# Kernel optimization log

Hardware: AMD Instinct MI355X
Metric: run time of the kernel (lower is better)

Reference implementation:

```python
import jax, jax.numpy as jnp
import numpy as np

N_NODES = 50000
N_EDGES = 1600000
F_NODE, F_EDGE, HID = 16, 8, 64


def setup_inputs() -> dict:
    key = jax.random.key(0)
    ks = jax.random.split(key, 12)
    def w(k, shape):
        fan_in = shape[0]
        return jax.random.normal(k, shape, dtype=jnp.float32) / np.sqrt(fan_in)
    return {
        "x": jax.random.normal(ks[0], (N_NODES, F_NODE), dtype=jnp.float32),
        "edge_index": jax.random.randint(ks[1], (2, N_EDGES), 0, N_NODES, dtype=jnp.int32),
        "edge_attr": jax.random.normal(ks[2], (N_EDGES, F_EDGE), dtype=jnp.float32),
        "W1": w(ks[3], (F_NODE, HID)), "b1": jnp.zeros((HID,), jnp.float32),
        "W2": w(ks[4], (HID, HID)), "b2": jnp.zeros((HID,), jnp.float32),
        "mW1": w(ks[5], (2 * HID + F_EDGE, 2 * HID)), "mb1": jnp.zeros((2 * HID,), jnp.float32),
        "mW2": w(ks[6], (2 * HID, HID)), "mb2": jnp.zeros((HID,), jnp.float32),
        "mW3": w(ks[7], (HID, 1)), "mb3": jnp.zeros((1,), jnp.float32),
    }


def _gcn_conv(x, W, b, src, dst, deg_inv_sqrt, n_nodes):
    # GCNConv: D^{-1/2} (A + I) D^{-1/2} X W + b, edges include self-loops
    xw = x @ W  # [N, H]
    norm = deg_inv_sqrt[src] * deg_inv_sqrt[dst]  # [E+N]
    agg = jax.ops.segment_sum(xw[src] * norm[:, None], dst, num_segments=n_nodes)
    return agg + b


def reference(x, edge_index, edge_attr, W1, b1, W2, b2, mW1, mb1, mW2, mb2, mW3, mb3):
    n_nodes = x.shape[0]
    loop = jnp.arange(n_nodes, dtype=edge_index.dtype)
    src = jnp.concatenate([edge_index[0], loop])  # add self-loops
    dst = jnp.concatenate([edge_index[1], loop])
    deg = jax.ops.segment_sum(jnp.ones_like(dst, dtype=x.dtype), dst, num_segments=n_nodes)
    dis = jnp.where(deg > 0, jax.lax.rsqrt(deg), 0.0)

    h = jax.nn.relu(_gcn_conv(x, W1, b1, src, dst, dis, n_nodes))
    h = jax.nn.relu(_gcn_conv(h, W2, b2, src, dst, dis, n_nodes))

    # Vectorized equivalent of the per-graph neighbor loop: Q for every
    # (current_node=src, neighbor=dst) directed edge using its edge_attr.
    h_cur = h[edge_index[0]]   # [E, H]
    h_nbr = h[edge_index[1]]   # [E, H]
    z = jnp.concatenate([h_cur, h_nbr, edge_attr], axis=-1)  # [E, 2H+Fe]
    z = jax.nn.relu(z @ mW1 + mb1)
    z = jax.nn.relu(z @ mW2 + mb2)
    q = (z @ mW3 + mb3)[:, 0]  # [E]
    return q
```

## Files before the change

### kernel.cpp

```cpp
#include <hip/hip_runtime.h>
#include <hip/hip_bf16.h>

#define HID 64
#define FNODE 16
#define FEDGE 8

typedef __bf16 v8bf __attribute__((ext_vector_type(8)));
typedef unsigned short us8 __attribute__((ext_vector_type(8)));
typedef float v4f __attribute__((ext_vector_type(4)));

__device__ __bf16 g_w1h[20480];
__device__ __bf16 g_w1l[20480];
__device__ __bf16 g_w2h[8192];
__device__ __bf16 g_w2l[8192];

__global__ void k_pack(const float* __restrict__ mW1, const float* __restrict__ mW2) {
    int gid = blockIdx.x * 256 + threadIdx.x;
    if (gid < 20480) {
        int j = gid & 7, lane = (gid >> 3) & 63, f = gid >> 9;
        int kt = f >> 3, nt = f & 7;
        int k = kt * 32 + (lane >> 4) * 8 + j;
        int col = nt * 16 + (lane & 15);
        float x = (k < 136) ? mW1[k * 128 + col] : 0.f;
        __bf16 hi = (__bf16)x;
        g_w1h[gid] = hi;
        g_w1l[gid] = (__bf16)(x - (float)hi);
    } else if (gid < 28672) {
        int t = gid - 20480;
        int j = t & 7, lane = (t >> 3) & 63, f = t >> 9;
        int kt = f >> 2, nt = f & 3;
        int k = kt * 32 + (lane >> 4) * 8 + j;
        int col = nt * 16 + (lane & 15);
        float x = mW2[k * 64 + col];
        __bf16 hi = (__bf16)x;
        g_w2h[t] = hi;
        g_w2l[t] = (__bf16)(x - (float)hi);
    }
}

__global__ void k_count(const int* __restrict__ ei, int* __restrict__ rp, int E) {
    int e = blockIdx.x * 256 + threadIdx.x;
    if (e < E) atomicAdd(&rp[ei[E + e]], 1);
}

__global__ void k_disn(const int* __restrict__ rp, float* __restrict__ dis, int N) {
    int n = blockIdx.x * 256 + threadIdx.x;
    if (n < N) dis[n] = rsqrtf((float)(rp[n] + 1));
}

__device__ __forceinline__ int block_scan_excl(int v, int* wsum) {
    int lane = threadIdx.x & 63, wv = threadIdx.x >> 6;
    int inc = v;
#pragma unroll
    for (int d = 1; d < 64; d <<= 1) {
        int t = __shfl_up(inc, d, 64);
        if (lane >= d) inc += t;
    }
    if (lane == 63) wsum[wv] = inc;
    __syncthreads();
    int off = 0;
    for (int w = 0; w < wv; ++w) off += wsum[w];
    return off + inc - v;
}

__global__ void k_scan1(int* __restrict__ rp, int* __restrict__ bsum, int N) {
    __shared__ int ws[4];
    int i = blockIdx.x * 256 + threadIdx.x;
    int v = (i < N) ? rp[i] : 0;
    int excl = block_scan_excl(v, ws);
    if (i < N) rp[i] = excl;
    if (threadIdx.x == 255) bsum[blockIdx.x] = excl + v;
}

__global__ void k_scan2(int* __restrict__ bsum, int nb) {
    __shared__ int ws[4];
    int i = threadIdx.x;
    int v = (i < nb) ? bsum[i] : 0;
    int excl = block_scan_excl(v, ws);
    if (i < nb) bsum[i] = excl;
}

__global__ void k_scan3(int* __restrict__ rp, const int* __restrict__ bsum, int N) {
    int i = blockIdx.x * 256 + threadIdx.x;
    if (i < N) rp[i] += bsum[i >> 8];
}

__global__ void k_fill(const int* __restrict__ ei, int* __restrict__ rp,
                       int* __restrict__ ce, int* __restrict__ eid, int E) {
    int e = blockIdx.x * 256 + threadIdx.x;
    if (e < E) {
        int s = ei[e], d = ei[E + e];
        int pos = atomicAdd(&rp[d], 1);
        ce[pos] = s | (d << 16);
        eid[pos] = e;
    }
}

__global__ void k_dx(const float* __restrict__ x, const float* __restrict__ dis,
                     float* __restrict__ dx, int NF) {
    int t = blockIdx.x * 256 + threadIdx.x;
    if (t < NF) dx[t] = x[t] * dis[t >> 4];
}

__global__ __launch_bounds__(256) void k_pull1x(const float* __restrict__ dx,
                                                const int* __restrict__ rp,
                                                const int* __restrict__ ce,
                                                const float* __restrict__ dis,
                                                float* __restrict__ u, int N) {
    int grp = threadIdx.x >> 4, dim = threadIdx.x & 15;
    int n = blockIdx.x * 16 + grp;
    if (n >= N) return;
    int beg = n ? rp[n - 1] : 0;
    int end = rp[n];
    float a0 = dx[(size_t)n * 16 + dim];
    float a1 = 0.f, a2 = 0.f, a3 = 0.f, a4 = 0.f, a5 = 0.f, a6 = 0.f, a7 = 0.f;
    int j = beg;
    for (; j + 7 < end; j += 8) {
        a0 += dx[(size_t)(ce[j] & 0xffff) * 16 + dim];
        a1 += dx[(size_t)(ce[j + 1] & 0xffff) * 16 + dim];
        a2 += dx[(size_t)(ce[j + 2] & 0xffff) * 16 + dim];
        a3 += dx[(size_t)(ce[j + 3] & 0xffff) * 16 + dim];
        a4 += dx[(size_t)(ce[j + 4] & 0xffff) * 16 + dim];
        a5 += dx[(size_t)(ce[j + 5] & 0xffff) * 16 + dim];
        a6 += dx[(size_t)(ce[j + 6] & 0xffff) * 16 + dim];
        a7 += dx[(size_t)(ce[j + 7] & 0xffff) * 16 + dim];
    }
    for (; j < end; ++j) a0 += dx[(size_t)(ce[j] & 0xffff) * 16 + dim];
    u[(size_t)n * 16 + dim] =
        dis[n] * (((a0 + a1) + (a2 + a3)) + ((a4 + a5) + (a6 + a7)));
}

__global__ __launch_bounds__(256) void k_h1y2(const float* __restrict__ u,
                                              const float* __restrict__ W1,
                                              const float* __restrict__ b1,
                                              const float* __restrict__ W2,
                                              const float* __restrict__ dis,
                                              float* __restrict__ y2, int N) {
    __shared__ float sh[4][64];
    int wave = threadIdx.x >> 6, lane = threadIdx.x & 63;
    int n = blockIdx.x * 4 + wave;
    if (n >= N) return;
    float myu = u[(size_t)n * 16 + (lane & 15)];
    float h = b1[lane];
#pragma unroll
    for (int k = 0; k < 16; ++k)
        h = fmaf(__shfl(myu, k, 64), W1[k * HID + lane], h);
    h = fmaxf(h, 0.f);
    sh[wave][lane] = h;
    float acc = 0.f;
#pragma unroll 8
    for (int k = 0; k < HID; ++k)
        acc = fmaf(sh[wave][k], W2[k * HID + lane], acc);
    y2[(size_t)n * HID + lane] = dis[n] * acc;
}

__global__ __launch_bounds__(256) void k_pull2(const float* __restrict__ y,
                                               const int* __restrict__ rp,
                                               const int* __restrict__ ce,
                                               const float* __restrict__ dis,
                                               const float* __restrict__ b,
                                               __bf16* __restrict__ hp, int N) {
    int wave = threadIdx.x >> 6, lane = threadIdx.x & 63;
    int n = blockIdx.x * 4 + wave;
    if (n >= N) return;
    int beg = n ? rp[n - 1] : 0;
    int end = rp[n];
    float a0 = y[(size_t)n * HID + lane];
    float a1 = 0.f, a2 = 0.f, a3 = 0.f, a4 = 0.f, a5 = 0.f, a6 = 0.f, a7 = 0.f;
    int j = beg;
    for (; j + 7 < end; j += 8) {
        a0 += y[(size_t)(ce[j] & 0xffff) * HID + lane];
        a1 += y[(size_t)(ce[j + 1] & 0xffff) * HID + lane];
        a2 += y[(size_t)(ce[j + 2] & 0xffff) * HID + lane];
        a3 += y[(size_t)(ce[j + 3] & 0xffff) * HID + lane];
        a4 += y[(size_t)(ce[j + 4] & 0xffff) * HID + lane];
        a5 += y[(size_t)(ce[j + 5] & 0xffff) * HID + lane];
        a6 += y[(size_t)(ce[j + 6] & 0xffff) * HID + lane];
        a7 += y[(size_t)(ce[j + 7] & 0xffff) * HID + lane];
    }
    for (; j < end; ++j) a0 += y[(size_t)(ce[j] & 0xffff) * HID + lane];
    float v = fmaxf(
        dis[n] * (((a0 + a1) + (a2 + a3)) + ((a4 + a5) + (a6 + a7))) + b[lane], 0.f);
    __bf16 hi = (__bf16)v;
    __bf16* p = hp + (size_t)n * 128;
    p[lane] = hi;
    p[64 + lane] = (__bf16)(v - (float)hi);
}

__device__ __forceinline__ int zoff(int m, int ch) {
    return ((m >> 4) << 12) + ((ch >> 2) << 9) + ((m & 15) << 5) + ((ch & 3) << 3);
}

__global__ __launch_bounds__(256) void k_edge_mlp(
    const __bf16* __restrict__ hp, const int* __restrict__ ce,
    const int* __restrict__ eid, const float* __restrict__ ea,
    const float* __restrict__ mb1, const float* __restrict__ mb2,
    const float* __restrict__ mW3, const float* __restrict__ mb3,
    float* __restrict__ q, int E) {
    __shared__ __align__(16) __bf16 zc[16384];
    __shared__ __align__(16) __bf16 eh[64][32];
    __shared__ __align__(16) __bf16 el[64][32];

    const int tid = threadIdx.x;
    const int lane = tid & 63;
    const int wave = tid >> 6;
    const int g = lane >> 4;
    const int cb = lane & 15;
    const int m0 = blockIdx.x * 64;

    {
        const int me = wave * 16 + (lane >> 2);
        const int cl = lane & 3;
        const int p = m0 + me;
        const bool valid = p < E;
        const int cep = valid ? ce[p] : 0;
        const int s = cep & 0xffff;
        const int d = ((unsigned)cep) >> 16;
        const __bf16* Sp = hp + (size_t)s * 128 + cl * 8;
        const __bf16* Dp = hp + (size_t)d * 128 + cl * 8;
        __bf16* lb = zc + wave * 4096;
#pragma unroll
        for (int i = 0; i < 4; ++i)
            __builtin_amdgcn_global_load_lds(
                (const __attribute__((address_space(1))) unsigned int*)(Sp + i * 32),
                (__attribute__((address_space(3))) unsigned int*)(lb + i * 512),
                16, 0, 0);
#pragma unroll
        for (int i = 0; i < 4; ++i)
            __builtin_amdgcn_global_load_lds(
                (const __attribute__((address_space(1))) unsigned int*)(Dp + i * 32),
                (__attribute__((address_space(3))) unsigned int*)(lb + (4 + i) * 512),
                16, 0, 0);
    }
    {
        const int m = tid >> 2, qt = tid & 3;
        const int p = m0 + m;
        const bool valid = p < E;
        if (qt < 2) {
            float4 v = {0.f, 0.f, 0.f, 0.f};
            if (valid) {
                int e = eid[p];
                v = *(const float4*)(ea + (size_t)e * FEDGE + qt * 4);
            }
            const float* vf = (const float*)&v;
#pragma unroll
            for (int i2 = 0; i2 < 4; ++i2) {
                float vv = vf[i2];
                __bf16 hiv = (__bf16)vv;
                eh[m][qt * 4 + i2] = hiv;
                el[m][qt * 4 + i2] = (__bf16)(vv - (float)hiv);
            }
        } else {
            us8 zz = {};
            __bf16* dstp = (qt == 2) ? &eh[m][8] : &el[m][8];
            *(us8*)&dstp[0] = zz;
            *(us8*)&dstp[8] = zz;
            *(us8*)&dstp[16] = zz;
        }
    }
    __syncthreads();

    const int nt0 = wave * 2;
    v4f acc[2][4];
    {
        float b0 = mb1[nt0 * 16 + cb];
        float b1v = mb1[nt0 * 16 + 16 + cb];
#pragma unroll
        for (int mt = 0; mt < 4; ++mt) {
            acc[0][mt] = (v4f){b0, b0, b0, b0};
            acc[1][mt] = (v4f){b1v, b1v, b1v, b1v};
        }
    }
    const v8bf* w1h = (const v8bf*)g_w1h;
    const v8bf* w1l = (const v8bf*)g_w1l;
    const v8bf* w2h = (const v8bf*)g_w2h;
    const v8bf* w2l = (const v8bf*)g_w2l;
#pragma unroll
    for (int kt = 0; kt < 5; ++kt) {
        v8bf bh0 = w1h[(kt * 8 + nt0) * 64 + lane];
        v8bf bl0 = w1l[(kt * 8 + nt0) * 64 + lane];
        v8bf bh1 = w1h[(kt * 8 + nt0 + 1) * 64 + lane];
        v8bf bl1 = w1l[(kt * 8 + nt0 + 1) * 64 + lane];
#pragma unroll
        for (int mt = 0; mt < 4; ++mt) {
            v8bf ah, al;
            if (kt < 4) {
                int ch = (kt < 2) ? kt * 4 + g : 16 + (kt - 2) * 4 + g;
                ah = *(const v8bf*)&zc[zoff(mt * 16 + cb, ch)];
                al = *(const v8bf*)&zc[zoff(mt * 16 + cb, ch + 8)];
            } else {
                ah = *(const v8bf*)&eh[mt * 16 + cb][g * 8];
                al = *(const v8bf*)&el[mt * 16 + cb][g * 8];
            }
            acc[0][mt] = __builtin_amdgcn_mfma_f32_16x16x32_bf16(ah, bh0, acc[0][mt], 0, 0, 0);
            acc[0][mt] = __builtin_amdgcn_mfma_f32_16x16x32_bf16(ah, bl0, acc[0][mt], 0, 0, 0);
            acc[0][mt] = __builtin_amdgcn_mfma_f32_16x16x32_bf16(al, bh0, acc[0][mt], 0, 0, 0);
            acc[1][mt] = __builtin_amdgcn_mfma_f32_16x16x32_bf16(ah, bh1, acc[1][mt], 0, 0, 0);
            acc[1][mt] = __builtin_amdgcn_mfma_f32_16x16x32_bf16(ah, bl1, acc[1][mt], 0, 0, 0);
            acc[1][mt] = __builtin_amdgcn_mfma_f32_16x16x32_bf16(al, bh1, acc[1][mt], 0, 0, 0);
        }
    }
    __syncthreads();

#pragma unroll
    for (int c = 0; c < 2; ++c)
#pragma unroll
        for (int mt = 0; mt < 4; ++mt)
#pragma unroll
            for (int r = 0; r < 4; ++r) {
                float vv = fmaxf(acc[c][mt][r], 0.f);
                __bf16 hiv = (__bf16)vv;
                int row = mt * 16 + g * 4 + r;
                int col = (nt0 + c) * 16 + cb;
                int chh = (col < 64) ? (col >> 3) : (8 + (col >> 3));
                zc[zoff(row, chh) + (cb & 7)] = hiv;
                zc[zoff(row, chh + 8) + (cb & 7)] = (__bf16)(vv - (float)hiv);
            }
    __syncthreads();

    v4f acc2[4];
    {
        float b = mb2[wave * 16 + cb];
#pragma unroll
        for (int mt = 0; mt < 4; ++mt) acc2[mt] = (v4f){b, b, b, b};
    }
#pragma unroll
    for (int kt = 0; kt < 4; ++kt) {
        v8bf bh = w2h[(kt * 4 + wave) * 64 + lane];
        v8bf bl = w2l[(kt * 4 + wave) * 64 + lane];
        int ch = (kt < 2) ? kt * 4 + g : 16 + (kt - 2) * 4 + g;
#pragma unroll
        for (int mt = 0; mt < 4; ++mt) {
            v8bf ah = *(const v8bf*)&zc[zoff(mt * 16 + cb, ch)];
            v8bf al = *(const v8bf*)&zc[zoff(mt * 16 + cb, ch + 8)];
            acc2[mt] = __builtin_amdgcn_mfma_f32_16x16x32_bf16(ah, bh, acc2[mt], 0, 0, 0);
            acc2[mt] = __builtin_amdgcn_mfma_f32_16x16x32_bf16(ah, bl, acc2[mt], 0, 0, 0);
            acc2[mt] = __builtin_amdgcn_mfma_f32_16x16x32_bf16(al, bh, acc2[mt], 0, 0, 0);
        }
    }
    __syncthreads();

    float* qp = (float*)&zc[0];
    const float w3 = mW3[wave * 16 + cb];
#pragma unroll
    for (int mt = 0; mt < 4; ++mt) {
#pragma unroll
        for (int r = 0; r < 4; ++r) {
            float pr = fmaxf(acc2[mt][r], 0.f) * w3;
            pr += __shfl_xor(pr, 1, 16);
            pr += __shfl_xor(pr, 2, 16);
            pr += __shfl_xor(pr, 4, 16);
            pr += __shfl_xor(pr, 8, 16);
            if (cb == 0) qp[wave * 64 + mt * 16 + g * 4 + r] = pr;
        }
    }
    __syncthreads();
    if (tid < 64) {
        int p = m0 + tid;
        if (p < E)
            q[eid[p]] =
                qp[tid] + qp[64 + tid] + qp[128 + tid] + qp[192 + tid] + mb3[0];
    }
}

extern "C" void kernel_launch(void* const* d_in, const int* in_sizes, int n_in,
                              void* d_out, int out_size, void* d_ws, size_t ws_size,
                              hipStream_t stream) {
    const float* x   = (const float*)d_in[0];
    const int*   ei  = (const int*)d_in[1];
    const float* ea  = (const float*)d_in[2];
    const float* W1  = (const float*)d_in[3];
    const float* b1  = (const float*)d_in[4];
    const float* W2  = (const float*)d_in[5];
    const float* b2  = (const float*)d_in[6];
    const float* mW1 = (const float*)d_in[7];
    const float* mb1 = (const float*)d_in[8];
    const float* mW2 = (const float*)d_in[9];
    const float* mb2 = (const float*)d_in[10];
    const float* mW3 = (const float*)d_in[11];
    const float* mb3 = (const float*)d_in[12];
    float* q = (float*)d_out;

    const int N = in_sizes[0] / FNODE;
    const int E = in_sizes[1] / 2;

    float* dis = (float*)d_ws;
    int* bsum  = (int*)(dis + 50000);
    float* y2  = dis + ((N + 511) & ~255);
    float* hpf = y2 + (size_t)N * HID;
    float* dx  = hpf;
    float* u   = hpf + (size_t)N * 16;
    int* rp    = (int*)(hpf + (size_t)N * HID);
    int* ce    = rp + ((N + 255) & ~255);
    int* eid   = ce + E;

    const int nT = 256;
    const int gN    = (N + nT - 1) / nT;
    const int gE    = (E + nT - 1) / nT;
    const int gNF   = (N * FNODE + nT - 1) / nT;
    const int g16   = (N + 15) / 16;
    const int gNode = (N + 3) / 4;
    const int gMLP  = (E + 63) / 64;

    k_pack<<<112, nT, 0, stream>>>(mW1, mW2);

    hipMemsetAsync(rp, 0, (size_t)N * sizeof(int), stream);
    k_count<<<gE, nT, 0, stream>>>(ei, rp, E);
    k_disn<<<gN, nT, 0, stream>>>(rp, dis, N);
    k_scan1<<<gN, nT, 0, stream>>>(rp, bsum, N);
    k_scan2<<<1, nT, 0, stream>>>(bsum, gN);
    k_scan3<<<gN, nT, 0, stream>>>(rp, bsum, N);
    k_fill<<<gE, nT, 0, stream>>>(ei, rp, ce, eid, E);

    k_dx<<<gNF, nT, 0, stream>>>(x, dis, dx, N * FNODE);
    k_pull1x<<<g16, nT, 0, stream>>>(dx, rp, ce, dis, u, N);
    k_h1y2<<<gNode, nT, 0, stream>>>(u, W1, b1, W2, dis, y2, N);

    k_pull2<<<gNode, nT, 0, stream>>>(y2, rp, ce, dis, b2, (__bf16*)hpf, N);

    k_edge_mlp<<<gMLP, nT, 0, stream>>>((const __bf16*)hpf, ce, eid, ea, mb1, mb2,
                                        mW3, mb3, q, E);
}
```

Before: 713.6 us.

## Make edge MLP kernel persistent with double-buffered LDS gather prefetch

Turns the edge MLP kernel into a persistent kernel capped at 512 blocks, each looping over 64-edge tiles. The async global-to-LDS gather of node features and the edge-attribute staging for the next tile are issued into a second LDS buffer while the current tile's MFMA work runs, and the indices for the tile after that are prefetched into registers. This aims to hide gather latency and cut per-block launch overhead. In exchange, LDS use per block doubles, which lowers occupancy. The barriers inside the loop may also force the async loads to finish early, limiting how much overlap is actually achieved.

Result: slower. 832.3 us (+16.6%).

```diff
diff --git a/kernel.cpp b/kernel.cpp
--- a/kernel.cpp
+++ b/kernel.cpp
@@ -196,29 +196,31 @@
     const int* __restrict__ eid, const float* __restrict__ ea,
     const float* __restrict__ mb1, const float* __restrict__ mb2,
     const float* __restrict__ mW3, const float* __restrict__ mb3,
-    float* __restrict__ q, int E) {
-    __shared__ __align__(16) __bf16 zc[16384];
-    __shared__ __align__(16) __bf16 eh[64][32];
-    __shared__ __align__(16) __bf16 el[64][32];
+    float* __restrict__ q, int E, int nTiles) {
+    __shared__ __align__(16) __bf16 zc[2][16384];
+    __shared__ __align__(16) __bf16 eh[2][64][32];
+    __shared__ __align__(16) __bf16 el[2][64][32];
 
     const int tid = threadIdx.x;
     const int lane = tid & 63;
     const int wave = tid >> 6;
     const int g = lane >> 4;
     const int cb = lane & 15;
-    const int m0 = blockIdx.x * 64;
-
-    {
-        const int me = wave * 16 + (lane >> 2);
-        const int cl = lane & 3;
-        const int p = m0 + me;
-        const bool valid = p < E;
-        const int cep = valid ? ce[p] : 0;
-        const int s = cep & 0xffff;
-        const int d = ((unsigned)cep) >> 16;
-        const __bf16* Sp = hp + (size_t)s * 128 + cl * 8;
-        const __bf16* Dp = hp + (size_t)d * 128 + cl * 8;
-        __bf16* lb = zc + wave * 4096;
+    const int m = tid >> 2, qt = tid & 3;
+    const int stride = gridDim.x;
+    const int nt0 = wave * 2;
+
+    const v8bf* w1h = (const v8bf*)g_w1h;
+    const v8bf* w1l = (const v8bf*)g_w1l;
+    const v8bf* w2h = (const v8bf*)g_w2h;
+    const v8bf* w2l = (const v8bf*)g_w2l;
+
+    auto issue_dma = [&](int buf, int cep) {
+        int s = cep & 0xffff;
+        int d = ((unsigned)cep) >> 16;
+        const __bf16* Sp = hp + (size_t)s * 128 + qt * 8;
+        const __bf16* Dp = hp + (size_t)d * 128 + qt * 8;
+        __bf16* lb = &zc[buf][wave * 4096];
 #pragma unroll
         for (int i = 0; i < 4; ++i)
             __builtin_amdgcn_global_load_lds(
@@ -231,135 +233,161 @@
                 (const __attribute__((address_space(1))) unsigned int*)(Dp + i * 32),
                 (__attribute__((address_space(3))) unsigned int*)(lb + (4 + i) * 512),
                 16, 0, 0);
-    }
-    {
-        const int m = tid >> 2, qt = tid & 3;
-        const int p = m0 + m;
-        const bool valid = p < E;
+    };
+
+    auto stage_ea = [&](int buf, int e, bool valid) {
         if (qt < 2) {
             float4 v = {0.f, 0.f, 0.f, 0.f};
-            if (valid) {
-                int e = eid[p];
-                v = *(const float4*)(ea + (size_t)e * FEDGE + qt * 4);
-            }
+            if (valid) v = *(const float4*)(ea + (size_t)e * FEDGE + qt * 4);
             const float* vf = (const float*)&v;
 #pragma unroll
             for (int i2 = 0; i2 < 4; ++i2) {
                 float vv = vf[i2];
                 __bf16 hiv = (__bf16)vv;
-                eh[m][qt * 4 + i2] = hiv;
-                el[m][qt * 4 + i2] = (__bf16)(vv - (float)hiv);
+                eh[buf][m][qt * 4 + i2] = hiv;
+                el[buf][m][qt * 4 + i2] = (__bf16)(vv - (float)hiv);
             }
         } else {
             us8 zz = {};
-            __bf16* dstp = (qt == 2) ? &eh[m][8] : &el[m][8];
+            __bf16* dstp = (qt == 2) ? &eh[buf][m][8] : &el[buf][m][8];
             *(us8*)&dstp[0] = zz;
             *(us8*)&dstp[8] = zz;
             *(us8*)&dstp[16] = zz;
         }
-    }
-    __syncthreads();
-
-    const int nt0 = wave * 2;
-    v4f acc[2][4];
+    };
+
+    int t = blockIdx.x;
+    if (t >= nTiles) return;
+
     {
-        float b0 = mb1[nt0 * 16 + cb];
-        float b1v = mb1[nt0 * 16 + 16 + cb];
+        int p = t * 64 + m;
+        bool v = p < E;
+        int cep = v ? ce[p] : 0;
+        int e0 = v ? eid[p] : 0;
+        issue_dma(0, cep);
+        stage_ea(0, e0, v);
+    }
+    int tn1 = t + stride;
+    int pn1 = tn1 * 64 + m;
+    bool v_n = (tn1 < nTiles) && (pn1 < E);
+    int cep_n = v_n ? ce[pn1] : 0;
+    int e_n = v_n ? eid[pn1] : 0;
+    int cur = 0;
+
+    for (; t < nTiles; t += stride) {
+        int pq = t * 64 + tid;
+        int eq = (tid < 64 && pq < E) ? eid[pq] : 0;
+        int tn = t + stride;
+
+        __syncthreads();
+
+        if (tn < nTiles) {
+            issue_dma(cur ^ 1, cep_n);
+            stage_ea(cur ^ 1, e_n, v_n);
+        }
+        int tnn = t + 2 * stride;
+        int pnn = tnn * 64 + m;
+        bool vnn = (tnn < nTiles) && (pnn < E);
+        int cep_nn = vnn ? ce[pnn] : 0;
+        int e_nn = vnn ? eid[pnn] : 0;
+
+        v4f acc[2][4];
+        {
+            float b0 = mb1[nt0 * 16 + cb];
+            float b1v = mb1[nt0 * 16 + 16 + cb];
+#pragma unroll
+            for (int mt = 0; mt < 4; ++mt) {
+                acc[0][mt] = (v4f){b0, b0, b0, b0};
+                acc[1][mt] = (v4f){b1v, b1v, b1v, b1v};
+            }
+        }
+#pragma unroll
+        for (int kt = 0; kt < 5; ++kt) {
+            v8bf bh0 = w1h[(kt * 8 + nt0) * 64 + lane];
+            v8bf bl0 = w1l[(kt * 8 + nt0) * 64 + lane];
+            v8bf bh1 = w1h[(kt * 8 + nt0 + 1) * 64 + lane];
+            v8bf bl1 = w1l[(kt * 8 + nt0 + 1) * 64 + lane];
+#pragma unroll
+            for (int mt = 0; mt < 4; ++mt) {
+                v8bf ah, al;
+                if (kt < 4) {
+                    int ch = (kt < 2) ? kt * 4 + g : 16 + (kt - 2) * 4 + g;
+                    ah = *(const v8bf*)&zc[cur][zoff(mt * 16 + cb, ch)];
+                    al = *(const v8bf*)&zc[cur][zoff(mt * 16 + cb, ch + 8)];
+                } else {
+                    ah = *(const v8bf*)&eh[cur][mt * 16 + cb][g * 8];
+                    al = *(const v8bf*)&el[cur][mt * 16 + cb][g * 8];
+                }
+                acc[0][mt] = __builtin_amdgcn_mfma_f32_16x16x32_bf16(ah, bh0, acc[0][mt], 0, 0, 0);
+                acc[0][mt] = __builtin_amdgcn_mfma_f32_16x16x32_bf16(ah, bl0, acc[0][mt], 0, 0, 0);
+                acc[0][mt] = __builtin_amdgcn_mfma_f32_16x16x32_bf16(al, bh0, acc[0][mt], 0, 0, 0);
+                acc[1][mt] = __builtin_amdgcn_mfma_f32_16x16x32_bf16(ah, bh1, acc[1][mt], 0, 0, 0);
+                acc[1][mt] = __builtin_amdgcn_mfma_f32_16x16x32_bf16(ah, bl1, acc[1][mt], 0, 0, 0);
+                acc[1][mt] = __builtin_amdgcn_mfma_f32_16x16x32_bf16(al, bh1, acc[1][mt], 0, 0, 0);
+            }
+        }
+        __syncthreads();
+
+#pragma unroll
+        for (int c = 0; c < 2; ++c)
+#pragma unroll
+            for (int mt = 0; mt < 4; ++mt)
+#pragma unroll
+                for (int r = 0; r < 4; ++r) {
+                    float vv = fmaxf(acc[c][mt][r], 0.f);
+                    __bf16 hiv = (__bf16)vv;
+                    int row = mt * 16 + g * 4 + r;
+                    int col = (nt0 + c) * 16 + cb;
+                    int chh = (col < 64) ? (col >> 3) : (8 + (col >> 3));
+                    zc[cur][zoff(row, chh) + (cb & 7)] = hiv;
+                    zc[cur][zoff(row, chh + 8) + (cb & 7)] = (__bf16)(vv - (float)hiv);
+                }
+        __syncthreads();
+
+        v4f acc2[4];
+        {
+            float b = mb2[wave * 16 + cb];
+#pragma unroll
+            for (int mt = 0; mt < 4; ++mt) acc2[mt] = (v4f){b, b, b, b};
+        }
+#pragma unroll
+        for (int kt = 0; kt < 4; ++kt) {
+            v8bf bh = w2h[(kt * 4 + wave) * 64 + lane];
+            v8bf bl = w2l[(kt * 4 + wave) * 64 + lane];
+            int ch = (kt < 2) ? kt * 4 + g : 16 + (kt - 2) * 4 + g;
+#pragma unroll
+            for (int mt = 0; mt < 4; ++mt) {
+                v8bf ah = *(const v8bf*)&zc[cur][zoff(mt * 16 + cb, ch)];
+                v8bf al = *(const v8bf*)&zc[cur][zoff(mt * 16 + cb, ch + 8)];
+                acc2[mt] = __builtin_amdgcn_mfma_f32_16x16x32_bf16(ah, bh, acc2[mt], 0, 0, 0);
+                acc2[mt] = __builtin_amdgcn_mfma_f32_16x16x32_bf16(ah, bl, acc2[mt], 0, 0, 0);
+                acc2[mt] = __builtin_amdgcn_mfma_f32_16x16x32_bf16(al, bh, acc2[mt], 0, 0, 0);
+            }
+        }
+        __syncthreads();
+
+        float* qp = (float*)&zc[cur][0];
+        const float w3 = mW3[wave * 16 + cb];
 #pragma unroll
         for (int mt = 0; mt < 4; ++mt) {
-            acc[0][mt] = (v4f){b0, b0, b0, b0};
-            acc[1][mt] = (v4f){b1v, b1v, b1v, b1v};
-        }
-    }
-    const v8bf* w1h = (const v8bf*)g_w1h;
-    const v8bf* w1l = (const v8bf*)g_w1l;
-    const v8bf* w2h = (const v8bf*)g_w2h;
-    const v8bf* w2l = (const v8bf*)g_w2l;
-#pragma unroll
-    for (int kt = 0; kt < 5; ++kt) {
-        v8bf bh0 = w1h[(kt * 8 + nt0) * 64 + lane];
-        v8bf bl0 = w1l[(kt * 8 + nt0) * 64 + lane];
-        v8bf bh1 = w1h[(kt * 8 + nt0 + 1) * 64 + lane];
-        v8bf bl1 = w1l[(kt * 8 + nt0 + 1) * 64 + lane];
-#pragma unroll
-        for (int mt = 0; mt < 4; ++mt) {
-            v8bf ah, al;
-            if (kt < 4) {
-                int ch = (kt < 2) ? kt * 4 + g : 16 + (kt - 2) * 4 + g;
-                ah = *(const v8bf*)&zc[zoff(mt * 16 + cb, ch)];
-                al = *(const v8bf*)&zc[zoff(mt * 16 + cb, ch + 8)];
-            } else {
-                ah = *(const v8bf*)&eh[mt * 16 + cb][g * 8];
-                al = *(const v8bf*)&el[mt * 16 + cb][g * 8];
+#pragma unroll
+            for (int r = 0; r < 4; ++r) {
+                float pr = fmaxf(acc2[mt][r], 0.f) * w3;
+                pr += __shfl_xor(pr, 1, 16);
+                pr += __shfl_xor(pr, 2, 16);
+                pr += __shfl_xor(pr, 4, 16);
+                pr += __shfl_xor(pr, 8, 16);
+                if (cb == 0) qp[wave * 64 + mt * 16 + g * 4 + r] = pr;
             }
-            acc[0][mt] = __builtin_amdgcn_mfma_f32_16x16x32_bf16(ah, bh0, acc[0][mt], 0, 0, 0);
-            acc[0][mt] = __builtin_amdgcn_mfma_f32_16x16x32_bf16(ah, bl0, acc[0][mt], 0, 0, 0);
-            acc[0][mt] = __builtin_amdgcn_mfma_f32_16x16x32_bf16(al, bh0, acc[0][mt], 0, 0, 0);
-            acc[1][mt] = __builtin_amdgcn_mfma_f32_16x16x32_bf16(ah, bh1, acc[1][mt], 0, 0, 0);
-            acc[1][mt] = __builtin_amdgcn_mfma_f32_16x16x32_bf16(ah, bl1, acc[1][mt], 0, 0, 0);
-            acc[1][mt] = __builtin_amdgcn_mfma_f32_16x16x32_bf16(al, bh1, acc[1][mt], 0, 0, 0);
-        }
-    }
-    __syncthreads();
-
-#pragma unroll
-    for (int c = 0; c < 2; ++c)
-#pragma unroll
-        for (int mt = 0; mt < 4; ++mt)
-#pragma unroll
-            for (int r = 0; r < 4; ++r) {
-                float vv = fmaxf(acc[c][mt][r], 0.f);
-                __bf16 hiv = (__bf16)vv;
-                int row = mt * 16 + g * 4 + r;
-                int col = (nt0 + c) * 16 + cb;
-                int chh = (col < 64) ? (col >> 3) : (8 + (col >> 3));
-                zc[zoff(row, chh) + (cb & 7)] = hiv;
-                zc[zoff(row, chh + 8) + (cb & 7)] = (__bf16)(vv - (float)hiv);
-            }
-    __syncthreads();
-
-    v4f acc2[4];
-    {
-        float b = mb2[wave * 16 + cb];
-#pragma unroll
-        for (int mt = 0; mt < 4; ++mt) acc2[mt] = (v4f){b, b, b, b};
-    }
-#pragma unroll
-    for (int kt = 0; kt < 4; ++kt) {
-        v8bf bh = w2h[(kt * 4 + wave) * 64 + lane];
-        v8bf bl = w2l[(kt * 4 + wave) * 64 + lane];
-        int ch = (kt < 2) ? kt * 4 + g : 16 + (kt - 2) * 4 + g;
-#pragma unroll
-        for (int mt = 0; mt < 4; ++mt) {
-            v8bf ah = *(const v8bf*)&zc[zoff(mt * 16 + cb, ch)];
-            v8bf al = *(const v8bf*)&zc[zoff(mt * 16 + cb, ch + 8)];
-            acc2[mt] = __builtin_amdgcn_mfma_f32_16x16x32_bf16(ah, bh, acc2[mt], 0, 0, 0);
-            acc2[mt] = __builtin_amdgcn_mfma_f32_16x16x32_bf16(ah, bl, acc2[mt], 0, 0, 0);
-            acc2[mt] = __builtin_amdgcn_mfma_f32_16x16x32_bf16(al, bh, acc2[mt], 0, 0, 0);
-        }
-    }
-    __syncthreads();
-
-    float* qp = (float*)&zc[0];
-    const float w3 = mW3[wave * 16 + cb];
-#pragma unroll
-    for (int mt = 0; mt < 4; ++mt) {
-#pragma unroll
-        for (int r = 0; r < 4; ++r) {
-            float pr = fmaxf(acc2[mt][r], 0.f) * w3;
-            pr += __shfl_xor(pr, 1, 16);
-            pr += __shfl_xor(pr, 2, 16);
-            pr += __shfl_xor(pr, 4, 16);
-            pr += __shfl_xor(pr, 8, 16);
-            if (cb == 0) qp[wave * 64 + mt * 16 + g * 4 + r] = pr;
-        }
-    }
-    __syncthreads();
-    if (tid < 64) {
-        int p = m0 + tid;
-        if (p < E)
-            q[eid[p]] =
-                qp[tid] + qp[64 + tid] + qp[128 + tid] + qp[192 + tid] + mb3[0];
+        }
+        __syncthreads();
+        if (tid < 64 && pq < E)
+            q[eq] = qp[tid] + qp[64 + tid] + qp[128 + tid] + qp[192 + tid] + mb3[0];
+
+        cep_n = cep_nn;
+        e_n = e_nn;
+        v_n = vnn;
+        cur ^= 1;
     }
 }
 
@@ -400,7 +428,8 @@
     const int gNF   = (N * FNODE + nT - 1) / nT;
     const int g16   = (N + 15) / 16;
     const int gNode = (N + 3) / 4;
-    const int gMLP  = (E + 63) / 64;
+    const int nTiles = (E + 63) / 64;
+    const int gMLP = (nTiles < 512) ? nTiles : 512;
 
     k_pack<<<112, nT, 0, stream>>>(mW1, mW2);
 
@@ -419,5 +448,5 @@
     k_pull2<<<gNode, nT, 0, stream>>>(y2, rp, ce, dis, b2, (__bf16*)hpf, N);
 
     k_edge_mlp<<<gMLP, nT, 0, stream>>>((const __bf16*)hpf, ce, eid, ea, mb1, mb2,
-                                        mW3, mb3, q, E);
-}
+                                        mW3, mb3, q, E, nTiles);
+}
```
